# Performance work log

Hardware: AMD Instinct MI355X
Metric: run time of the kernel (lower is better)

The kernel has to match this reference:

```python
import jax, jax.numpy as jnp
import numpy as np

RCR = 5.2
RCA = 3.5
ETA_R = np.array([16.0], np.float32)                      # (1,)
SHF_R = (0.9 + 0.26875 * np.arange(16)).astype(np.float32)  # (16,)
ETA_A = np.array([8.0], np.float32)                       # (1,)
ZETA = np.array([32.0], np.float32)                       # (1,)
SHF_A = np.array([0.9, 1.55, 2.2, 2.85], np.float32)      # (4,)
SHF_Z = (np.pi / 16 + (np.pi / 8) * np.arange(8)).astype(np.float32)  # (8,)
NUM_SPECIES = 4
C, A = 16, 64
EPS = 1e-8  # torch cosine_similarity eps

# unordered species-pair index table: (s1, s2) -> triu pair id (10 pairs for 4 species)
_tbl = np.zeros((NUM_SPECIES, NUM_SPECIES), np.int32)
_k = 0
for _a in range(NUM_SPECIES):
    for _b in range(_a, NUM_SPECIES):
        _tbl[_a, _b] = _k
        _tbl[_b, _a] = _k
        _k += 1
PAIR_TABLE = jnp.asarray(_tbl)
NUM_SP_PAIRS = _k  # 10

IDX_I, IDX_J = np.triu_indices(A, k=1)  # neighbor pair combinations, P = A*(A-1)/2


def _cutoff_cosine(d, rc):
    return jnp.where(d <= rc, 0.5 * jnp.cos(np.pi * d / rc) + 0.5, 0.0)


def setup_inputs() -> dict:
    key = jax.random.key(0)
    k1, k2 = jax.random.split(key)
    species = jax.random.randint(k1, (C, A), 0, NUM_SPECIES)
    # spread atoms over a realistic box so distances span the cutoffs
    coordinates = jax.random.normal(k2, (C, A, 3), dtype=jnp.float32) * 4.0
    return {"species": species, "coordinates": coordinates}


def reference(species, coordinates):
    f32 = coordinates.dtype
    # vec[c,i,j,:] = R_i - R_j  (matches coordinates.unsqueeze(2)-unsqueeze(1))
    vec = coordinates[:, :, None, :] - coordinates[:, None, :, :]  # (C,A,A,3)
    i_idx = jnp.arange(A)
    # valid neighbor: not self, not padding (species == -1)
    valid = (i_idx[:, None] != i_idx[None, :])[None] & (species[:, None, :] != -1)  # (C,A,A)
    vec_safe = jnp.where(valid[..., None], vec, 1.0)
    d = jnp.linalg.norm(vec_safe, axis=-1)          # (C,A,A)
    d = jnp.where(valid, d, RCR + 1.0)

    # ---- radial subAEV terms: 0.25 * exp(-EtaR (d - ShfR)^2) * fc ----
    fc = _cutoff_cosine(d, RCR)                      # (C,A,A)
    shf_r = jnp.asarray(SHF_R)
    eta_r = jnp.asarray(ETA_R)[0]
    rt = 0.25 * jnp.exp(-eta_r * (d[..., None] - shf_r) ** 2) * fc[..., None]  # (C,A,A,16)
    rt = rt * valid[..., None].astype(f32)
    onehot_s = (species[:, :, None] == jnp.arange(NUM_SPECIES)).astype(f32)  # (C,A,S)
    radial_aev = jnp.einsum('cijr,cjs->cisr', rt, onehot_s)  # (C,A,S,16)
    radial_aev = radial_aev.reshape(C, A, NUM_SPECIES * SHF_R.size)

    # ---- angular subAEV terms over neighbor pairs ----
    v1 = vec[:, :, IDX_I, :]                         # (C,A,P,3)
    v2 = vec[:, :, IDX_J, :]
    pair_valid = valid[:, :, IDX_I] & valid[:, :, IDX_J]  # (C,A,P)
    v1s = jnp.where(pair_valid[..., None], v1, 1.0)
    v2s = jnp.where(pair_valid[..., None], v2, 1.0)
    d1 = jnp.linalg.norm(v1s, axis=-1)
    d2 = jnp.linalg.norm(v2s, axis=-1)
    d1 = jnp.where(pair_valid, d1, RCA + 1.0)
    d2 = jnp.where(pair_valid, d2, RCA + 1.0)
    cos_ang = 0.95 * jnp.sum(v1s * v2s, -1) / (jnp.maximum(d1, EPS) * jnp.maximum(d2, EPS))
    angles = jnp.arccos(cos_ang)                     # |cos|<=0.95 so safe
    fcj1 = _cutoff_cosine(d1, RCA)
    fcj2 = _cutoff_cosine(d2, RCA)
    # broadcast layout (..., EtaA=1, Zeta=1, ShfA=4, ShfZ=8) -> flatten to 32
    shf_a = jnp.asarray(SHF_A).reshape(1, 1, 4, 1)
    shf_z = jnp.asarray(SHF_Z).reshape(1, 1, 1, 8)
    zeta = jnp.asarray(ZETA)[0]
    eta_a = jnp.asarray(ETA_A)[0]
    ang = angles[..., None, None, None, None]        # (C,A,P,1,1,1,1)
    dm = ((d1 + d2) / 2)[..., None, None, None, None]
    factor1 = ((1 + jnp.cos(ang - shf_z)) / 2) ** zeta
    factor2 = jnp.exp(-eta_a * (dm - shf_a) ** 2)
    at = 2 * factor1 * factor2 * fcj1[..., None, None, None, None] * fcj2[..., None, None, None, None]
    P = IDX_I.size
    at = at.reshape(C, A, P, 32) * pair_valid[..., None].astype(f32)  # (C,A,P,32)

    # species-pair one-hot over the P neighbor pairs
    sp1 = jnp.clip(species[:, IDX_I], 0, NUM_SPECIES - 1)  # (C,P); padding masked by pair_valid
    sp2 = jnp.clip(species[:, IDX_J], 0, NUM_SPECIES - 1)
    pid = PAIR_TABLE[sp1, sp2]                       # (C,P)
    onehot_p = (pid[..., None] == jnp.arange(NUM_SP_PAIRS)).astype(f32)  # (C,P,10)
    angular_aev = jnp.einsum('cipz,cpt->citz', at, onehot_p)  # (C,A,10,32)
    angular_aev = angular_aev.reshape(C, A, NUM_SP_PAIRS * 32)

    return jnp.concatenate([radial_aev, angular_aev], axis=-1)  # (C,A,384)
```

## Files before the change

kernel.cpp:

```cpp
#include <hip/hip_runtime.h>
#include <hip/hip_bf16.h>

#define RCR 5.2f
#define RCA 3.5f
#define PI_F 3.14159265358979323846f

__global__ __launch_bounds__(384)
void aev_kernel(const int* __restrict__ species,
                const float* __restrict__ coords,
                float* __restrict__ out)
{
    const int blk = blockIdx.x;
    const int c   = blk >> 6;
    const int i   = blk & 63;
    const int tid = threadIdx.x;

    __shared__ float sxx[64], syy[64], szz[64];
    __shared__ int   ssp[64];
    __shared__ float nrx[64], nry[64], nrz[64];
    __shared__ float nd[64], ninv[64], nfcR[64], nfcA[64];
    __shared__ int   alist[64];
    __shared__ int   acount;
    __shared__ int   pairjk[2016];

    if (tid == 0) acount = 0;
    if (tid < 64) {
        const int j = tid;
        const int base = (c * 64 + j) * 3;
        sxx[j] = coords[base + 0];
        syy[j] = coords[base + 1];
        szz[j] = coords[base + 2];
        ssp[j] = species[c * 64 + j];
    }
    __syncthreads();

    if (tid < 64) {
        const int j = tid;
        float rx = sxx[i] - sxx[j];
        float ry = syy[i] - syy[j];
        float rz = szz[i] - szz[j];
        float d  = sqrtf(rx*rx + ry*ry + rz*rz);
        bool valid = (j != i) && (ssp[j] != -1);
        float fr = 0.f, fa = 0.f, inv = 0.f;
        if (valid) {
            inv = 1.0f / fmaxf(d, 1e-8f);
            if (d <= RCR) fr = 0.5f * __cosf(PI_F * d * (1.0f/RCR)) + 0.5f;
            if (d <= RCA) {
                fa = 0.5f * __cosf(PI_F * d * (1.0f/RCA)) + 0.5f;
                int pos = atomicAdd(&acount, 1);
                alist[pos] = j;
            }
        }
        nrx[j] = rx; nry[j] = ry; nrz[j] = rz;
        nd[j] = d; ninv[j] = inv; nfcR[j] = fr; nfcA[j] = fa;
    }
    __syncthreads();

    const int n = acount;
    if (tid < n) {
        int a = tid;
        int base = a * (n - 1) - (a * (a - 1)) / 2;
        int ja = alist[a];
        for (int b = a + 1; b < n; ++b)
            pairjk[base + (b - a - 1)] = (ja << 8) | alist[b];
    }
    __syncthreads();

    const int np = (n * (n - 1)) >> 1;
    const long ob = (long)(c * 64 + i) * 384;

    if (tid < 64) {
        const int s = tid >> 4, r = tid & 15;
        const float shf = 0.9f + 0.26875f * (float)r;
        float acc = 0.f;
        for (int j = 0; j < 64; ++j) {
            if (ssp[j] == s) {
                float u = nd[j] - shf;
                acc += 0.25f * __expf(-16.f * u * u) * nfcR[j];
            }
        }
        out[ob + tid] = acc;
    } else {
        const int slot = tid - 64;
        const int pid  = slot >> 5;
        const int aa   = (slot >> 3) & 3;
        const int z    = slot & 7;
        const float shfa = 0.9f + 0.65f * (float)aa;
        const float shfz = PI_F / 16.f + (PI_F / 8.f) * (float)z;
        const float czv = __cosf(shfz);
        const float szv = __sinf(shfz);
        float acc = 0.f;
        for (int p = 0; p < np; ++p) {
            int jk = pairjk[p];
            int j = jk >> 8, k = jk & 255;
            int s1 = ssp[j], s2 = ssp[k];
            int mn = min(s1, s2), mx = max(s1, s2);
            int ppid = ((mn * (7 - mn)) >> 1) + mx;
            float dot = nrx[j]*nrx[k] + nry[j]*nry[k] + nrz[j]*nrz[k];
            float ca  = 0.95f * dot * ninv[j] * ninv[k];
            float sa  = sqrtf(fmaxf(0.f, 1.f - ca * ca));
            float dm  = 0.5f * (nd[j] + nd[k]);
            float fprod = 2.f * nfcA[j] * nfcA[k];
            float cd = ca * czv + sa * szv;
            float t  = 0.5f + 0.5f * cd;
            t = t * t; t = t * t; t = t * t; t = t * t; t = t * t;
            float u  = dm - shfa;
            float f2 = __expf(-8.f * u * u);
            float val = t * f2 * fprod;
            acc += (ppid == pid) ? val : 0.f;
        }
        out[ob + 64 + slot] = acc;
    }
}

extern "C" void kernel_launch(void* const* d_in, const int* in_sizes, int n_in,
                              void* d_out, int out_size, void* d_ws, size_t ws_size,
                              hipStream_t stream) {
    const int* species   = (const int*)d_in[0];
    const float* coords  = (const float*)d_in[1];
    float* out           = (float*)d_out;
    aev_kernel<<<dim3(16 * 64), dim3(384), 0, stream>>>(species, coords, out);
}
```

Baseline: 72.27 us.

## Rewrite AEV kernel as single-wavefront with compacted neighbor lists and atomic accumulation

Shrinks each block to one 64-lane wavefront. Wave shuffles and ballot/popcount replace the shared staging and atomic list building. Radial terms now loop only over neighbors inside the cutoff. Angular terms compute each neighbor pair once per (shfa, shfz) slot instead of once for each of the 10 species-pair lanes, then scatter into the species-pair bin with LDS atomics. The aim is to remove the 10x redundant angular work and the extra barriers. The cost is fewer threads per block and atomic contention on shared accumulators.

```diff
diff --git a/kernel.cpp b/kernel.cpp
--- a/kernel.cpp
+++ b/kernel.cpp
@@ -1,11 +1,10 @@
 #include <hip/hip_runtime.h>
-#include <hip/hip_bf16.h>
 
 #define RCR 5.2f
 #define RCA 3.5f
 #define PI_F 3.14159265358979323846f
 
-__global__ __launch_bounds__(384)
+__global__ __launch_bounds__(64)
 void aev_kernel(const int* __restrict__ species,
                 const float* __restrict__ coords,
                 float* __restrict__ out)
@@ -13,111 +12,112 @@
     const int blk = blockIdx.x;
     const int c   = blk >> 6;
     const int i   = blk & 63;
-    const int tid = threadIdx.x;
+    const int l   = threadIdx.x;
 
-    __shared__ float sxx[64], syy[64], szz[64];
-    __shared__ int   ssp[64];
-    __shared__ float nrx[64], nry[64], nrz[64];
-    __shared__ float nd[64], ninv[64], nfcR[64], nfcA[64];
-    __shared__ int   alist[64];
-    __shared__ int   acount;
-    __shared__ int   pairjk[2016];
+    const int gbase = (c * 64 + l) * 3;
+    float x = coords[gbase + 0];
+    float y = coords[gbase + 1];
+    float z = coords[gbase + 2];
+    int  sp = species[c * 64 + l];
 
-    if (tid == 0) acount = 0;
-    if (tid < 64) {
-        const int j = tid;
-        const int base = (c * 64 + j) * 3;
-        sxx[j] = coords[base + 0];
-        syy[j] = coords[base + 1];
-        szz[j] = coords[base + 2];
-        ssp[j] = species[c * 64 + j];
+    float xi = __shfl(x, i);
+    float yi = __shfl(y, i);
+    float zi = __shfl(z, i);
+
+    float rx = xi - x, ry = yi - y, rz = zi - z;
+    float d  = sqrtf(rx * rx + ry * ry + rz * rz);
+    bool valid  = (l != i) && (sp != -1);
+    bool rvalid = valid && (d <= RCR);
+    bool avalid = valid && (d <= RCA);
+
+    __shared__ float cx[64], cy[64], cz[64], cd_[64], cinv[64], cfa[64];
+    __shared__ int   csp[64];
+    __shared__ float rd[64], rfc[64];
+    __shared__ int   rsp[64];
+    __shared__ int   pairab[1953];
+    __shared__ float acc[320];
+
+    for (int t = l; t < 320; t += 64) acc[t] = 0.f;
+
+    unsigned long long rmask = __ballot(rvalid);
+    unsigned long long amask = __ballot(avalid);
+    const int nr = __popcll(rmask);
+    const int n  = __popcll(amask);
+    const unsigned long long below = (l == 0) ? 0ull : (~0ull >> (64 - l));
+
+    if (rvalid) {
+        int pos = __popcll(rmask & below);
+        rd[pos]  = d;
+        rfc[pos] = 0.5f * __cosf(PI_F * d * (1.0f / RCR)) + 0.5f;
+        rsp[pos] = sp;
+    }
+    if (avalid) {
+        int pos = __popcll(amask & below);
+        cx[pos] = rx; cy[pos] = ry; cz[pos] = rz;
+        cd_[pos]  = d;
+        cinv[pos] = 1.0f / fmaxf(d, 1e-8f);
+        cfa[pos]  = 0.5f * __cosf(PI_F * d * (1.0f / RCA)) + 0.5f;
+        csp[pos]  = sp;
+    }
+    if (l < n) {
+        int a = l;
+        int base = a * (n - 1) - (a * (a - 1)) / 2;
+        for (int b = a + 1; b < n; ++b)
+            pairab[base + (b - a - 1)] = (a << 6) | b;
     }
     __syncthreads();
 
-    if (tid < 64) {
-        const int j = tid;
-        float rx = sxx[i] - sxx[j];
-        float ry = syy[i] - syy[j];
-        float rz = szz[i] - szz[j];
-        float d  = sqrtf(rx*rx + ry*ry + rz*rz);
-        bool valid = (j != i) && (ssp[j] != -1);
-        float fr = 0.f, fa = 0.f, inv = 0.f;
-        if (valid) {
-            inv = 1.0f / fmaxf(d, 1e-8f);
-            if (d <= RCR) fr = 0.5f * __cosf(PI_F * d * (1.0f/RCR)) + 0.5f;
-            if (d <= RCA) {
-                fa = 0.5f * __cosf(PI_F * d * (1.0f/RCA)) + 0.5f;
-                int pos = atomicAdd(&acount, 1);
-                alist[pos] = j;
-            }
+    const int   s   = l >> 4;
+    const float shf = 0.9f + 0.26875f * (float)(l & 15);
+    float racc = 0.f;
+    for (int m = 0; m < nr; ++m) {
+        float dd   = rd[m] - shf;
+        float term = 0.25f * __expf(-16.f * dd * dd) * rfc[m];
+        racc += (rsp[m] == s) ? term : 0.f;
+    }
+
+    const int   sub  = l & 31;
+    const float shfa = 0.9f + 0.65f * (float)(sub >> 3);
+    const float shfz = PI_F / 16.f + (PI_F / 8.f) * (float)(sub & 7);
+    const float czv  = __cosf(shfz);
+    const float szv  = __sinf(shfz);
+    const int   np   = (n * (n - 1)) >> 1;
+    const int   half = l >> 5;
+    for (int p0 = 0; p0 < np; p0 += 2) {
+        int p = p0 + half;
+        if (p < np) {
+            int ab = pairab[p];
+            int a = ab >> 6, b = ab & 63;
+            float dot = cx[a] * cx[b] + cy[a] * cy[b] + cz[a] * cz[b];
+            float ca  = 0.95f * dot * cinv[a] * cinv[b];
+            float sa  = sqrtf(fmaxf(0.f, 1.f - ca * ca));
+            float dm  = 0.5f * (cd_[a] + cd_[b]);
+            float fprod = 2.f * cfa[a] * cfa[b];
+            int s1 = csp[a], s2 = csp[b];
+            int mn = min(s1, s2), mx = max(s1, s2);
+            int pid = ((mn * (7 - mn)) >> 1) + mx;
+            float cdz = ca * czv + sa * szv;
+            float t = 0.5f + 0.5f * cdz;
+            t = t * t; t = t * t; t = t * t; t = t * t; t = t * t;
+            float u = dm - shfa;
+            float val = t * __expf(-8.f * u * u) * fprod;
+            atomicAdd(&acc[pid * 32 + sub], val);
         }
-        nrx[j] = rx; nry[j] = ry; nrz[j] = rz;
-        nd[j] = d; ninv[j] = inv; nfcR[j] = fr; nfcA[j] = fa;
     }
     __syncthreads();
 
-    const int n = acount;
-    if (tid < n) {
-        int a = tid;
-        int base = a * (n - 1) - (a * (a - 1)) / 2;
-        int ja = alist[a];
-        for (int b = a + 1; b < n; ++b)
-            pairjk[base + (b - a - 1)] = (ja << 8) | alist[b];
-    }
-    __syncthreads();
-
-    const int np = (n * (n - 1)) >> 1;
-    const long ob = (long)(c * 64 + i) * 384;
-
-    if (tid < 64) {
-        const int s = tid >> 4, r = tid & 15;
-        const float shf = 0.9f + 0.26875f * (float)r;
-        float acc = 0.f;
-        for (int j = 0; j < 64; ++j) {
-            if (ssp[j] == s) {
-                float u = nd[j] - shf;
-                acc += 0.25f * __expf(-16.f * u * u) * nfcR[j];
-            }
-        }
-        out[ob + tid] = acc;
-    } else {
-        const int slot = tid - 64;
-        const int pid  = slot >> 5;
-        const int aa   = (slot >> 3) & 3;
-        const int z    = slot & 7;
-        const float shfa = 0.9f + 0.65f * (float)aa;
-        const float shfz = PI_F / 16.f + (PI_F / 8.f) * (float)z;
-        const float czv = __cosf(shfz);
-        const float szv = __sinf(shfz);
-        float acc = 0.f;
-        for (int p = 0; p < np; ++p) {
-            int jk = pairjk[p];
-            int j = jk >> 8, k = jk & 255;
-            int s1 = ssp[j], s2 = ssp[k];
-            int mn = min(s1, s2), mx = max(s1, s2);
-            int ppid = ((mn * (7 - mn)) >> 1) + mx;
-            float dot = nrx[j]*nrx[k] + nry[j]*nry[k] + nrz[j]*nrz[k];
-            float ca  = 0.95f * dot * ninv[j] * ninv[k];
-            float sa  = sqrtf(fmaxf(0.f, 1.f - ca * ca));
-            float dm  = 0.5f * (nd[j] + nd[k]);
-            float fprod = 2.f * nfcA[j] * nfcA[k];
-            float cd = ca * czv + sa * szv;
-            float t  = 0.5f + 0.5f * cd;
-            t = t * t; t = t * t; t = t * t; t = t * t; t = t * t;
-            float u  = dm - shfa;
-            float f2 = __expf(-8.f * u * u);
-            float val = t * f2 * fprod;
-            acc += (ppid == pid) ? val : 0.f;
-        }
-        out[ob + 64 + slot] = acc;
-    }
+    const long ob = (long)blk * 384;
+    out[ob + l] = racc;
+    #pragma unroll
+    for (int t = 0; t < 5; ++t)
+        out[ob + 64 + t * 64 + l] = acc[t * 64 + l];
 }
 
 extern "C" void kernel_launch(void* const* d_in, const int* in_sizes, int n_in,
                               void* d_out, int out_size, void* d_ws, size_t ws_size,
                               hipStream_t stream) {
-    const int* species   = (const int*)d_in[0];
-    const float* coords  = (const float*)d_in[1];
-    float* out           = (float*)d_out;
-    aev_kernel<<<dim3(16 * 64), dim3(384), 0, stream>>>(species, coords, out);
+    const int* species  = (const int*)d_in[0];
+    const float* coords = (const float*)d_in[1];
+    float* out          = (float*)d_out;
+    aev_kernel<<<dim3(16 * 64), dim3(64), 0, stream>>>(species, coords, out);
 }
```

Result: faster. 66.22 us (median of 2 runs) (-8.4%).
